# Kernel tuning notes

Hardware: AMD Instinct MI355X
Metric: run time of the kernel (lower is better)

Reference implementation:

```python
import jax, jax.numpy as jnp
import numpy as np

HIDDEN = 1024
HEADS = 16
HEAD_DIM = HIDDEN // HEADS
GAMMA = 0.5
B, S = 2, 2048


def setup_inputs() -> dict:
    key = jax.random.key(0)
    ks = jax.random.split(key, 9)
    sc = 1.0 / np.sqrt(HIDDEN)
    x = jax.random.normal(ks[0], (B, S, HIDDEN), dtype=jnp.float32)
    attn_mask = jnp.zeros((S, S), dtype=bool)  # True = masked; all-False here
    Wq = jax.random.normal(ks[1], (HIDDEN, HIDDEN), dtype=jnp.float32) * sc
    bq = jnp.zeros((HIDDEN,), dtype=jnp.float32)
    Wk = jax.random.normal(ks[2], (HIDDEN, HIDDEN), dtype=jnp.float32) * sc
    bk = jnp.zeros((HIDDEN,), dtype=jnp.float32)
    Wv = jax.random.normal(ks[3], (HIDDEN, HIDDEN), dtype=jnp.float32) * sc
    bv = jnp.zeros((HIDDEN,), dtype=jnp.float32)
    Wo = jax.random.normal(ks[4], (HIDDEN, HIDDEN), dtype=jnp.float32) * sc
    bo = jnp.zeros((HIDDEN,), dtype=jnp.float32)
    return {"x": x, "attn_mask": attn_mask, "Wq": Wq, "bq": bq,
            "Wk": Wk, "bk": bk, "Wv": Wv, "bv": bv, "Wo": Wo, "bo": bo}


def reference(x, attn_mask, Wq, bq, Wk, bk, Wv, bv, Wo, bo):
    Bn, Sn, _ = x.shape
    # projections (torch Linear: x @ W.T + b), reshape to [B, H, S, Dh]
    def proj(W, b):
        y = x @ W.T + b
        return y.reshape(Bn, Sn, HEADS, HEAD_DIM).transpose(0, 2, 1, 3)
    q, k, v = proj(Wq, bq), proj(Wk, bk), proj(Wv, bv)
    scores = jnp.einsum('bhqd,bhkd->bhqk', q, k) / np.sqrt(HEAD_DIM)
    # diversity bias: cosine similarity of raw x (F.normalize eps=1e-12)
    normed = x / jnp.maximum(jnp.linalg.norm(x, axis=-1, keepdims=True), 1e-12)
    sim = jnp.einsum('bqd,bkd->bqk', normed, normed)
    scores = scores - GAMMA * sim[:, None, :, :]
    scores = jnp.where(attn_mask[None, None, :, :], -jnp.inf, scores)
    probs = jax.nn.softmax(scores, axis=-1)
    ctx = jnp.einsum('bhqk,bhkd->bhqd', probs, v)
    ctx = ctx.transpose(0, 2, 1, 3).reshape(Bn, Sn, HIDDEN)
    return ctx @ Wo.T + bo
```

## Files before the change

### kernel.cpp

```cpp
#include <hip/hip_runtime.h>

#define HID 1024
#define SEQ 2048
#define NB 2
#define NH 16
#define HD 64

#define C1 0.1803368801111204f
#define C2 0.7213475204444817f

typedef __attribute__((ext_vector_type(8))) short bf16x8;
typedef __attribute__((ext_vector_type(8))) unsigned short u16x8;
typedef __attribute__((ext_vector_type(4))) float f32x4;

__device__ __forceinline__ unsigned short f2bf(float f) {
  unsigned u = __builtin_bit_cast(unsigned, f);
  u += 0x7fffu + ((u >> 16) & 1u);
  return (unsigned short)(u >> 16);
}
__device__ __forceinline__ float bf2f(unsigned short u) {
  return __builtin_bit_cast(float, ((unsigned)u) << 16);
}

#define GLOAD16(gsrc, ldst)                                                     \
  __builtin_amdgcn_global_load_lds(                                             \
      (const __attribute__((address_space(1))) void*)(gsrc),                    \
      (__attribute__((address_space(3))) void*)(ldst), 16, 0, 0)

__global__ __launch_bounds__(256) void prep_kernel(
    const float* __restrict__ x,
    const float* __restrict__ Wq, const float* __restrict__ Wk,
    const float* __restrict__ Wv, const float* __restrict__ Wo,
    unsigned short* __restrict__ Wb,
    unsigned short* __restrict__ xb, unsigned short* __restrict__ nxb) {
  int tid = threadIdx.x;
  if (blockIdx.x < 2048) {
    int i = blockIdx.x * 256 + tid;
    const int per = (HID * HID) / 8;
    int m = i / per;
    const float* sp = (m == 0) ? Wq : (m == 1) ? Wk : (m == 2) ? Wv : Wo;
    int j = (i - m * per) * 8;
    const float4* p = reinterpret_cast<const float4*>(sp + j);
    float4 a = p[0], b = p[1];
    u16x8 o;
    o[0] = f2bf(a.x); o[1] = f2bf(a.y); o[2] = f2bf(a.z); o[3] = f2bf(a.w);
    o[4] = f2bf(b.x); o[5] = f2bf(b.y); o[6] = f2bf(b.z); o[7] = f2bf(b.w);
    *reinterpret_cast<u16x8*>(Wb + (size_t)i * 8) = o;
  } else {
    int row = blockIdx.x - 2048;
    const float4 v = reinterpret_cast<const float4*>(x + (size_t)row * HID)[tid];
    float ss = v.x * v.x + v.y * v.y + v.z * v.z + v.w * v.w;
#pragma unroll
    for (int off = 32; off; off >>= 1) ss += __shfl_xor(ss, off, 64);
    __shared__ float wsum[4];
    if ((tid & 63) == 0) wsum[tid >> 6] = ss;
    __syncthreads();
    float tot = wsum[0] + wsum[1] + wsum[2] + wsum[3];
    float inv = 1.0f / fmaxf(sqrtf(tot), 1e-12f);
    ushort4 a, b;
    a.x = f2bf(v.x); a.y = f2bf(v.y); a.z = f2bf(v.z); a.w = f2bf(v.w);
    b.x = f2bf(v.x * inv); b.y = f2bf(v.y * inv);
    b.z = f2bf(v.z * inv); b.w = f2bf(v.w * inv);
    reinterpret_cast<ushort4*>(xb  + (size_t)row * HID)[tid] = a;
    reinterpret_cast<ushort4*>(nxb + (size_t)row * HID)[tid] = b;
  }
}

__global__ __launch_bounds__(256) void mega_gemm(
    const unsigned short* __restrict__ xb, const unsigned short* __restrict__ nxb,
    const unsigned short* __restrict__ Wb,
    unsigned short* __restrict__ QK, unsigned short* __restrict__ VT,
    unsigned short* __restrict__ D2,
    const float* __restrict__ bq, const float* __restrict__ bk,
    const float* __restrict__ bv, const unsigned char* __restrict__ mask) {
  const int K = HID;
  int bid = blockIdx.x;
  int mode, m0, n0;
  const unsigned short *A, *B;
  size_t zoff = 0;
  if (bid < 512) {
    mode = 0; m0 = (bid >> 4) * 128; n0 = (bid & 15) * 128;
    A = xb; B = Wb;
  } else if (bid < 768) {
    mode = 3; int t = bid - 512; m0 = (t >> 5) * 128; n0 = (t & 31) * 128;
    A = Wb + (size_t)2 * HID * HID; B = xb;
  } else {
    mode = 1; int t = bid - 768; int z = 0;
    if (t >= 136) { z = 1; t -= 136; }
    int a = (int)((sqrtf(8.0f * t + 1.0f) - 1.0f) * 0.5f);
    while (a * (a + 1) / 2 > t) a--;
    while ((a + 1) * (a + 2) / 2 <= t) a++;
    int bI = t - a * (a + 1) / 2;
    m0 = bI * 128; n0 = a * 128;
    A = nxb + (size_t)z * SEQ * HID; B = A;
    zoff = (size_t)z * SEQ * SEQ;
  }

  __shared__ __align__(16) unsigned short As[128 * 32];
  __shared__ __align__(16) unsigned short Bs[128 * 32];
  int tid = threadIdx.x, lane = tid & 63, wid = tid >> 6;
  int g = lane >> 4, lr = lane & 15;
  int wr = wid >> 1, wc = wid & 1;
  const unsigned short* Ab = A + (size_t)(m0 + wid * 32 + (lane >> 2)) * K + (lane & 3) * 8;
  const unsigned short* Bb = B + (size_t)(n0 + wid * 32 + (lane >> 2)) * K + (lane & 3) * 8;
  unsigned short* la = As + wid * 1024;
  unsigned short* lb = Bs + wid * 1024;
  f32x4 acc[4][4] = {};
  for (int k0 = 0; k0 < K; k0 += 32) {
    GLOAD16(Ab + k0, la);
    GLOAD16(Ab + 16 * K + k0, la + 512);
    GLOAD16(Bb + k0, lb);
    GLOAD16(Bb + 16 * K + k0, lb + 512);
    __syncthreads();
    bf16x8 af[4], bfr[4];
#pragma unroll
    for (int i = 0; i < 4; i++) {
      af[i]  = *reinterpret_cast<const bf16x8*>(&As[(wr * 64 + i * 16 + lr) * 32 + g * 8]);
      bfr[i] = *reinterpret_cast<const bf16x8*>(&Bs[(wc * 64 + i * 16 + lr) * 32 + g * 8]);
    }
#pragma unroll
    for (int i = 0; i < 4; i++)
#pragma unroll
      for (int j = 0; j < 4; j++)
        acc[i][j] = __builtin_amdgcn_mfma_f32_16x16x32_bf16(af[i], bfr[j], acc[i][j], 0, 0, 0);
    __syncthreads();
  }
#pragma unroll
  for (int i = 0; i < 4; i++)
#pragma unroll
    for (int j = 0; j < 4; j++) {
      int col = n0 + wc * 64 + j * 16 + lr;
#pragma unroll
      for (int r = 0; r < 4; r++) {
        int row = m0 + wr * 64 + i * 16 + 4 * g + r;
        float v = acc[i][j][r];
        if (mode == 0) {
          const float* bp = (col < 1024) ? bq : bk;
          QK[(size_t)row * 2048 + col] = f2bf(v + bp[col & 1023]);
        } else if (mode == 3) {
          VT[(size_t)row * 4096 + col] = f2bf(v + bv[row]);
        } else {
          float t1 = -C2 * v + (mask[(size_t)row * SEQ + col] ? -1e30f : 0.0f);
          D2[zoff + (size_t)row * SEQ + col] = f2bf(t1);
          if (m0 != n0) {
            float t2 = -C2 * v + (mask[(size_t)col * SEQ + row] ? -1e30f : 0.0f);
            D2[zoff + (size_t)col * SEQ + row] = f2bf(t2);
          }
        }
      }
    }
}

__global__ __launch_bounds__(256) void gemm_out(
    const unsigned short* __restrict__ A, const unsigned short* __restrict__ B,
    float* __restrict__ C, const float* __restrict__ b0) {
  const int K = HID;
  __shared__ __align__(16) unsigned short As[128 * 32];
  __shared__ __align__(16) unsigned short Bs[128 * 32];
  int tid = threadIdx.x, lane = tid & 63, wid = tid >> 6;
  int g = lane >> 4, lr = lane & 15;
  int wr = wid >> 1, wc = wid & 1;
  int m0 = blockIdx.y * 128, n0 = blockIdx.x * 128;
  const unsigned short* Ab = A + (size_t)(m0 + wid * 32 + (lane >> 2)) * K + (lane & 3) * 8;
  const unsigned short* Bb = B + (size_t)(n0 + wid * 32 + (lane >> 2)) * K + (lane & 3) * 8;
  unsigned short* la = As + wid * 1024;
  unsigned short* lb = Bs + wid * 1024;
  f32x4 acc[4][4] = {};
  for (int k0 = 0; k0 < K; k0 += 32) {
    GLOAD16(Ab + k0, la);
    GLOAD16(Ab + 16 * K + k0, la + 512);
    GLOAD16(Bb + k0, lb);
    GLOAD16(Bb + 16 * K + k0, lb + 512);
    __syncthreads();
    bf16x8 af[4], bfr[4];
#pragma unroll
    for (int i = 0; i < 4; i++) {
      af[i]  = *reinterpret_cast<const bf16x8*>(&As[(wr * 64 + i * 16 + lr) * 32 + g * 8]);
      bfr[i] = *reinterpret_cast<const bf16x8*>(&Bs[(wc * 64 + i * 16 + lr) * 32 + g * 8]);
    }
#pragma unroll
    for (int i = 0; i < 4; i++)
#pragma unroll
      for (int j = 0; j < 4; j++)
        acc[i][j] = __builtin_amdgcn_mfma_f32_16x16x32_bf16(af[i], bfr[j], acc[i][j], 0, 0, 0);
    __syncthreads();
  }
#pragma unroll
  for (int i = 0; i < 4; i++)
#pragma unroll
    for (int j = 0; j < 4; j++) {
      int col = n0 + wc * 64 + j * 16 + lr;
#pragma unroll
      for (int r = 0; r < 4; r++) {
        int row = m0 + wr * 64 + i * 16 + 4 * g + r;
        C[(size_t)row * HID + col] = acc[i][j][r] + b0[col];
      }
    }
}

__global__ __launch_bounds__(256, 4) void flash_kernel(
    const unsigned short* __restrict__ QK,
    const unsigned short* __restrict__ VT,
    const unsigned short* __restrict__ D2,
    unsigned short* __restrict__ ctxb) {
  int h = blockIdx.x, qt = blockIdx.y, b = blockIdx.z;
  int tid = threadIdx.x, wid = tid >> 6, lane = tid & 63;
  int g = lane >> 4, lr = lane & 15;
  __shared__ __align__(16) unsigned short Ks[2][64 * 64];
  __shared__ __align__(16) unsigned short Vt[2][64 * 64];
  const size_t ld = 2 * HID;
  const size_t bS = (size_t)b * SEQ;
  const int qbase = qt * 64 + wid * 16;

  const unsigned short* qp = QK + (bS + qbase + lr) * ld + h * HD + g * 8;
  bf16x8 qf0 = *reinterpret_cast<const bf16x8*>(qp);
  bf16x8 qf1 = *reinterpret_cast<const bf16x8*>(qp + 32);

  const int p0 = wid * 16 + (lane >> 3);
  const int key0 = ((p0 >> 5) & 1) * 32 + (((p0 >> 2) & 3) << 3)
                 + ((p0 >> 4) & 1) * 4 + (p0 & 3);
  const unsigned short* gK0 = QK + (bS + key0) * ld + HID + h * HD
                              + (((lane & 7) ^ (lane >> 3)) << 3);
  const unsigned short* gK1 = gK0 + 16 * ld;

  const unsigned short* gV0 = VT + (size_t)(h * HD + wid * 16 + (lane >> 3)) * (2 * SEQ)
                              + bS + (((lane & 7) ^ (lane >> 3)) << 3);
  const unsigned short* gV1 = gV0 + (size_t)8 * (2 * SEQ);

  const unsigned short* bD = D2 + (size_t)b * SEQ * SEQ
                             + (size_t)(qbase + lr) * SEQ + 8 * g;

  GLOAD16(gK0, &Ks[0][wid * 1024]);
  GLOAD16(gK1, &Ks[0][wid * 1024 + 512]);
  GLOAD16(gV0, &Vt[0][wid * 1024]);
  GLOAD16(gV1, &Vt[0][wid * 1024 + 512]);
  ushort4 bvc[4];
  bvc[0] = *reinterpret_cast<const ushort4*>(bD + 0);
  bvc[1] = *reinterpret_cast<const ushort4*>(bD + 4);
  bvc[2] = *reinterpret_cast<const ushort4*>(bD + 32);
  bvc[3] = *reinterpret_cast<const ushort4*>(bD + 36);
  __syncthreads();

  f32x4 acc[4] = {};
  f32x4 rsacc = {};
  const int kb0 = lr * 64 + ((g ^ (lr & 7)) << 3);
  bf16x8 ones;
#pragma unroll
  for (int i = 0; i < 8; i++) ones[i] = 0x3F80;

  for (int kt = 0; kt < 32; ++kt) {
    const int cb = kt & 1;
    const unsigned short* ks = &Ks[cb][0];
    const unsigned short* vt = &Vt[cb][0];
    ushort4 bvn[4];
    if (kt < 31) {
      GLOAD16(gK0 + (size_t)(kt + 1) * 64 * ld, &Ks[cb ^ 1][wid * 1024]);
      GLOAD16(gK1 + (size_t)(kt + 1) * 64 * ld, &Ks[cb ^ 1][wid * 1024 + 512]);
      GLOAD16(gV0 + (kt + 1) * 64, &Vt[cb ^ 1][wid * 1024]);
      GLOAD16(gV1 + (kt + 1) * 64, &Vt[cb ^ 1][wid * 1024 + 512]);
      const unsigned short* bn = bD + (kt + 1) * 64;
      bvn[0] = *reinterpret_cast<const ushort4*>(bn + 0);
      bvn[1] = *reinterpret_cast<const ushort4*>(bn + 4);
      bvn[2] = *reinterpret_cast<const ushort4*>(bn + 32);
      bvn[3] = *reinterpret_cast<const ushort4*>(bn + 36);
    }

    f32x4 s[4];
    __builtin_amdgcn_s_setprio(1);
#pragma unroll
    for (int kc = 0; kc < 4; kc++) {
      bf16x8 kf0 = *reinterpret_cast<const bf16x8*>(ks + kc * 1024 + kb0);
      bf16x8 kf1 = *reinterpret_cast<const bf16x8*>(ks + kc * 1024 + (kb0 ^ 32));
      f32x4 z = {};
      z = __builtin_amdgcn_mfma_f32_16x16x32_bf16(kf0, qf0, z, 0, 0, 0);
      s[kc] = __builtin_amdgcn_mfma_f32_16x16x32_bf16(kf1, qf1, z, 0, 0, 0);
    }
    __builtin_amdgcn_s_setprio(0);

    bf16x8 pa[2];
#pragma unroll
    for (int c2 = 0; c2 < 2; c2++) {
      float p0f = exp2f(fmaf(s[2 * c2][0], C1, bf2f(bvc[2 * c2].x)));
      float p1f = exp2f(fmaf(s[2 * c2][1], C1, bf2f(bvc[2 * c2].y)));
      float p2f = exp2f(fmaf(s[2 * c2][2], C1, bf2f(bvc[2 * c2].z)));
      float p3f = exp2f(fmaf(s[2 * c2][3], C1, bf2f(bvc[2 * c2].w)));
      float p4f = exp2f(fmaf(s[2 * c2 + 1][0], C1, bf2f(bvc[2 * c2 + 1].x)));
      float p5f = exp2f(fmaf(s[2 * c2 + 1][1], C1, bf2f(bvc[2 * c2 + 1].y)));
      float p6f = exp2f(fmaf(s[2 * c2 + 1][2], C1, bf2f(bvc[2 * c2 + 1].z)));
      float p7f = exp2f(fmaf(s[2 * c2 + 1][3], C1, bf2f(bvc[2 * c2 + 1].w)));
      uint4 W;
      W.x = __builtin_amdgcn_perm(__builtin_bit_cast(unsigned, p1f),
                                  __builtin_bit_cast(unsigned, p0f), 0x07060302u);
      W.y = __builtin_amdgcn_perm(__builtin_bit_cast(unsigned, p3f),
                                  __builtin_bit_cast(unsigned, p2f), 0x07060302u);
      W.z = __builtin_amdgcn_perm(__builtin_bit_cast(unsigned, p5f),
                                  __builtin_bit_cast(unsigned, p4f), 0x07060302u);
      W.w = __builtin_amdgcn_perm(__builtin_bit_cast(unsigned, p7f),
                                  __builtin_bit_cast(unsigned, p6f), 0x07060302u);
      pa[c2] = __builtin_bit_cast(bf16x8, W);
    }

    __builtin_amdgcn_s_setprio(1);
#pragma unroll
    for (int c2 = 0; c2 < 2; c2++) {
      rsacc = __builtin_amdgcn_mfma_f32_16x16x32_bf16(pa[c2], ones, rsacc, 0, 0, 0);
#pragma unroll
      for (int df = 0; df < 4; df++) {
        bf16x8 vf = *reinterpret_cast<const bf16x8*>(
            vt + (df * 16 + lr) * 64 + (((4 * c2 + g) ^ (lr & 7)) << 3));
        acc[df] = __builtin_amdgcn_mfma_f32_16x16x32_bf16(pa[c2], vf, acc[df], 0, 0, 0);
      }
    }
    __builtin_amdgcn_s_setprio(0);

    if (kt < 31) {
      bvc[0] = bvn[0]; bvc[1] = bvn[1]; bvc[2] = bvn[2]; bvc[3] = bvn[3];
    }
    __syncthreads();
  }
  float l0 = 1.0f / rsacc[0], l1 = 1.0f / rsacc[1];
  float l2 = 1.0f / rsacc[2], l3 = 1.0f / rsacc[3];
  unsigned short* op = ctxb + (bS + qbase + 4 * g) * HID + h * HD + lr;
#pragma unroll
  for (int df = 0; df < 4; df++) {
    op[0 * HID + df * 16] = f2bf(acc[df][0] * l0);
    op[1 * HID + df * 16] = f2bf(acc[df][1] * l1);
    op[2 * HID + df * 16] = f2bf(acc[df][2] * l2);
    op[3 * HID + df * 16] = f2bf(acc[df][3] * l3);
  }
}

extern "C" void kernel_launch(void* const* d_in, const int* in_sizes, int n_in,
                              void* d_out, int out_size, void* d_ws, size_t ws_size,
                              hipStream_t stream) {
  const float* x = (const float*)d_in[0];
  const unsigned char* mask = (const unsigned char*)d_in[1];
  const float* Wq = (const float*)d_in[2];
  const float* bq = (const float*)d_in[3];
  const float* Wk = (const float*)d_in[4];
  const float* bk = (const float*)d_in[5];
  const float* Wv = (const float*)d_in[6];
  const float* bv = (const float*)d_in[7];
  const float* Wo = (const float*)d_in[8];
  const float* bo = (const float*)d_in[9];
  float* out = (float*)d_out;

  char* ws = (char*)d_ws;
  const size_t MiB = 1024 * 1024;
  unsigned short* xb  = (unsigned short*)(ws + 0 * MiB);
  unsigned short* nxb = (unsigned short*)(ws + 8 * MiB);
  unsigned short* Wb  = (unsigned short*)(ws + 16 * MiB);
  unsigned short* QK  = (unsigned short*)(ws + 24 * MiB);
  unsigned short* VT  = (unsigned short*)(ws + 40 * MiB);
  unsigned short* D2  = (unsigned short*)(ws + 48 * MiB);
  unsigned short* ctx = (unsigned short*)(ws + 64 * MiB);

  prep_kernel<<<6144, 256, 0, stream>>>(x, Wq, Wk, Wv, Wo, Wb, xb, nxb);
  mega_gemm<<<1040, 256, 0, stream>>>(xb, nxb, Wb, QK, VT, D2, bq, bk, bv, mask);
  flash_kernel<<<dim3(NH, SEQ / 64, NB), 256, 0, stream>>>(QK, VT, D2, ctx);
  gemm_out<<<dim3(8, 32), 256, 0, stream>>>(
      ctx, Wb + (size_t)3 * HID * HID, out, bo);
}
```

Before: 196.3 us.

## Triple-buffer GEMM K-loop with async prefetch and XCD-aware block remap

Replaces the single-buffered GEMM K-loop in mega_gemm and gemm_out with a three-stage LDS ring. Direct-to-LDS loads are issued two tiles ahead and gated by explicit vmcnt waits, so global memory latency overlaps with MFMA work instead of stalling at each barrier. Block IDs are also remapped across the 8 XCDs, and the projection and out-projection tiles are traversed column-major so that blocks sharing weight or activation tiles run on the same XCD and reuse its L2. The cost is triple the LDS footprint, which can lower occupancy. Correctness now depends on the hand-counted vmcnt values matching the number of loads the GLOAD16 macro issues.

```diff
diff --git a/kernel.cpp b/kernel.cpp
--- a/kernel.cpp
+++ b/kernel.cpp
@@ -66,6 +66,46 @@
   }
 }
 
+#define ISSUE_TILE(kk, bf)                                                      \
+  do {                                                                          \
+    GLOAD16(Ab + (kk) * 32, &As[bf][lw]);                                       \
+    GLOAD16(Ab + 16 * K + (kk) * 32, &As[bf][lw + 512]);                        \
+    GLOAD16(Bb + (kk) * 32, &Bs[bf][lw]);                                       \
+    GLOAD16(Bb + 16 * K + (kk) * 32, &Bs[bf][lw + 512]);                        \
+  } while (0)
+
+#define GEMM_K_LOOP                                                             \
+  ISSUE_TILE(0, 0);                                                             \
+  ISSUE_TILE(1, 1);                                                             \
+  int buf = 0;                                                                  \
+  for (int kk = 0; kk < 32; ++kk) {                                             \
+    if (kk + 2 < 32) {                                                          \
+      int nb = buf == 0 ? 2 : buf - 1;                                          \
+      ISSUE_TILE(kk + 2, nb);                                                   \
+    }                                                                           \
+    if (kk < 30)       asm volatile("s_waitcnt vmcnt(8)" ::: "memory");         \
+    else if (kk == 30) asm volatile("s_waitcnt vmcnt(4)" ::: "memory");         \
+    else               asm volatile("s_waitcnt vmcnt(0)" ::: "memory");         \
+    __builtin_amdgcn_s_barrier();                                               \
+    const unsigned short* Ar = &As[buf][0];                                     \
+    const unsigned short* Br = &Bs[buf][0];                                     \
+    bf16x8 af[4], bfr[4];                                                       \
+    _Pragma("unroll")                                                           \
+    for (int i = 0; i < 4; i++) {                                               \
+      af[i]  = *reinterpret_cast<const bf16x8*>(&Ar[(wr * 64 + i * 16 + lr) * 32 + g * 8]); \
+      bfr[i] = *reinterpret_cast<const bf16x8*>(&Br[(wc * 64 + i * 16 + lr) * 32 + g * 8]); \
+    }                                                                           \
+    _Pragma("unroll")                                                           \
+    for (int i = 0; i < 4; i++)                                                 \
+      _Pragma("unroll")                                                         \
+      for (int j = 0; j < 4; j++)                                               \
+        acc[i][j] = __builtin_amdgcn_mfma_f32_16x16x32_bf16(af[i], bfr[j], acc[i][j], 0, 0, 0); \
+    __builtin_amdgcn_sched_barrier(0);                                          \
+    asm volatile("s_waitcnt lgkmcnt(0)" ::: "memory");                          \
+    __builtin_amdgcn_s_barrier();                                               \
+    buf = buf == 2 ? 0 : buf + 1;                                               \
+  }
+
 __global__ __launch_bounds__(256) void mega_gemm(
     const unsigned short* __restrict__ xb, const unsigned short* __restrict__ nxb,
     const unsigned short* __restrict__ Wb,
@@ -74,12 +114,12 @@
     const float* __restrict__ bq, const float* __restrict__ bk,
     const float* __restrict__ bv, const unsigned char* __restrict__ mask) {
   const int K = HID;
-  int bid = blockIdx.x;
+  int bid = (blockIdx.x & 7) * 130 + (blockIdx.x >> 3);
   int mode, m0, n0;
   const unsigned short *A, *B;
   size_t zoff = 0;
   if (bid < 512) {
-    mode = 0; m0 = (bid >> 4) * 128; n0 = (bid & 15) * 128;
+    mode = 0; n0 = (bid >> 5) * 128; m0 = (bid & 31) * 128;
     A = xb; B = Wb;
   } else if (bid < 768) {
     mode = 3; int t = bid - 512; m0 = (t >> 5) * 128; n0 = (t & 31) * 128;
@@ -96,35 +136,18 @@
     zoff = (size_t)z * SEQ * SEQ;
   }
 
-  __shared__ __align__(16) unsigned short As[128 * 32];
-  __shared__ __align__(16) unsigned short Bs[128 * 32];
+  __shared__ __align__(16) unsigned short As[3][128 * 32];
+  __shared__ __align__(16) unsigned short Bs[3][128 * 32];
   int tid = threadIdx.x, lane = tid & 63, wid = tid >> 6;
   int g = lane >> 4, lr = lane & 15;
   int wr = wid >> 1, wc = wid & 1;
   const unsigned short* Ab = A + (size_t)(m0 + wid * 32 + (lane >> 2)) * K + (lane & 3) * 8;
   const unsigned short* Bb = B + (size_t)(n0 + wid * 32 + (lane >> 2)) * K + (lane & 3) * 8;
-  unsigned short* la = As + wid * 1024;
-  unsigned short* lb = Bs + wid * 1024;
+  const int lw = wid * 1024;
+
   f32x4 acc[4][4] = {};
-  for (int k0 = 0; k0 < K; k0 += 32) {
-    GLOAD16(Ab + k0, la);
-    GLOAD16(Ab + 16 * K + k0, la + 512);
-    GLOAD16(Bb + k0, lb);
-    GLOAD16(Bb + 16 * K + k0, lb + 512);
-    __syncthreads();
-    bf16x8 af[4], bfr[4];
-#pragma unroll
-    for (int i = 0; i < 4; i++) {
-      af[i]  = *reinterpret_cast<const bf16x8*>(&As[(wr * 64 + i * 16 + lr) * 32 + g * 8]);
-      bfr[i] = *reinterpret_cast<const bf16x8*>(&Bs[(wc * 64 + i * 16 + lr) * 32 + g * 8]);
-    }
-#pragma unroll
-    for (int i = 0; i < 4; i++)
-#pragma unroll
-      for (int j = 0; j < 4; j++)
-        acc[i][j] = __builtin_amdgcn_mfma_f32_16x16x32_bf16(af[i], bfr[j], acc[i][j], 0, 0, 0);
-    __syncthreads();
-  }
+  GEMM_K_LOOP
+
 #pragma unroll
   for (int i = 0; i < 4; i++)
 #pragma unroll
@@ -155,36 +178,20 @@
     const unsigned short* __restrict__ A, const unsigned short* __restrict__ B,
     float* __restrict__ C, const float* __restrict__ b0) {
   const int K = HID;
-  __shared__ __align__(16) unsigned short As[128 * 32];
-  __shared__ __align__(16) unsigned short Bs[128 * 32];
+  __shared__ __align__(16) unsigned short As[3][128 * 32];
+  __shared__ __align__(16) unsigned short Bs[3][128 * 32];
   int tid = threadIdx.x, lane = tid & 63, wid = tid >> 6;
   int g = lane >> 4, lr = lane & 15;
   int wr = wid >> 1, wc = wid & 1;
-  int m0 = blockIdx.y * 128, n0 = blockIdx.x * 128;
+  int bid = (blockIdx.x & 7) * 32 + (blockIdx.x >> 3);
+  int n0 = (bid >> 5) * 128, m0 = (bid & 31) * 128;
   const unsigned short* Ab = A + (size_t)(m0 + wid * 32 + (lane >> 2)) * K + (lane & 3) * 8;
   const unsigned short* Bb = B + (size_t)(n0 + wid * 32 + (lane >> 2)) * K + (lane & 3) * 8;
-  unsigned short* la = As + wid * 1024;
-  unsigned short* lb = Bs + wid * 1024;
+  const int lw = wid * 1024;
+
   f32x4 acc[4][4] = {};
-  for (int k0 = 0; k0 < K; k0 += 32) {
-    GLOAD16(Ab + k0, la);
-    GLOAD16(Ab + 16 * K + k0, la + 512);
-    GLOAD16(Bb + k0, lb);
-    GLOAD16(Bb + 16 * K + k0, lb + 512);
-    __syncthreads();
-    bf16x8 af[4], bfr[4];
-#pragma unroll
-    for (int i = 0; i < 4; i++) {
-      af[i]  = *reinterpret_cast<const bf16x8*>(&As[(wr * 64 + i * 16 + lr) * 32 + g * 8]);
-      bfr[i] = *reinterpret_cast<const bf16x8*>(&Bs[(wc * 64 + i * 16 + lr) * 32 + g * 8]);
-    }
-#pragma unroll
-    for (int i = 0; i < 4; i++)
-#pragma unroll
-      for (int j = 0; j < 4; j++)
-        acc[i][j] = __builtin_amdgcn_mfma_f32_16x16x32_bf16(af[i], bfr[j], acc[i][j], 0, 0, 0);
-    __syncthreads();
-  }
+  GEMM_K_LOOP
+
 #pragma unroll
   for (int i = 0; i < 4; i++)
 #pragma unroll
@@ -358,6 +365,6 @@
   prep_kernel<<<6144, 256, 0, stream>>>(x, Wq, Wk, Wv, Wo, Wb, xb, nxb);
   mega_gemm<<<1040, 256, 0, stream>>>(xb, nxb, Wb, QK, VT, D2, bq, bk, bv, mask);
   flash_kernel<<<dim3(NH, SEQ / 64, NB), 256, 0, stream>>>(QK, VT, D2, ctx);
-  gemm_out<<<dim3(8, 32), 256, 0, stream>>>(
+  gemm_out<<<256, 256, 0, stream>>>(
       ctx, Wb + (size_t)3 * HID * HID, out, bo);
 }
```

Result: slower. 238.4 us (+21.5%).
